# Performance work log

Hardware: AMD Instinct MI355X
Metric: run time of the kernel (lower is better)

Reference implementation:

```python
import jax, jax.numpy as jnp
import numpy as np

VOCAB, EMB, HID, OUT = 32000, 512, 1024, 2
B, T = 64, 512


def setup_inputs() -> dict:
    key = jax.random.key(0)
    ks = jax.random.split(key, 12)
    def xavier(k, shape):
        fan_in, fan_out = shape
        lim = np.sqrt(6.0 / (fan_in + fan_out)).astype(np.float32)
        return jax.random.uniform(k, shape, jnp.float32, -lim, lim)
    x = jax.random.randint(ks[0], (B, T), 0, VOCAB, dtype=jnp.int32)
    emb = jax.random.uniform(ks[1], (VOCAB, EMB), jnp.float32, -0.1, 0.1)
    inp = {
        "x": x,
        "emb": emb,
        "Wxi": xavier(ks[2], (EMB, HID)), "Whi": xavier(ks[3], (HID, HID)), "bi": jnp.zeros((HID,), jnp.float32),
        "Wxf": xavier(ks[4], (EMB, HID)), "Whf": xavier(ks[5], (HID, HID)), "bf": jnp.zeros((HID,), jnp.float32),
        "Wxc": xavier(ks[6], (EMB, HID)), "Whc": xavier(ks[7], (HID, HID)), "bc": jnp.zeros((HID,), jnp.float32),
        "Wxo": xavier(ks[8], (EMB, HID)), "Who": xavier(ks[9], (HID, HID)), "bo": jnp.zeros((HID,), jnp.float32),
        "Why": xavier(ks[10], (HID, OUT)), "by": jnp.zeros((OUT,), jnp.float32),
    }
    return inp


def reference(x, emb, Wxi, Whi, bi, Wxf, Whf, bf, Wxc, Whc, bc, Wxo, Who, bo, Why, by):
    # Embedding lookup: [B, T, E]
    xe = emb[x]
    # Precompute input projections for all 4 gates in one batched contraction each.
    # Stack Wx matrices -> [E, 4H]; gates_x: [T, B, 4H] (time-major for scan)
    Wx = jnp.concatenate([Wxi, Wxf, Wxc, Wxo], axis=1)          # [E, 4H]
    Wh = jnp.concatenate([Whi, Whf, Whc, Who], axis=1)          # [H, 4H]
    b = jnp.concatenate([bi, bf, bc, bo], axis=0)               # [4H]
    gates_x = jnp.einsum('bte,eg->tbg', xe, Wx)                  # [T, B, 4H]
    H = Whi.shape[0]

    def step(carry, gx):
        h, c = carry
        g = gx + h @ Wh + b                                      # [B, 4H]
        i = jax.nn.sigmoid(g[:, 0 * H:1 * H])
        f = jax.nn.sigmoid(g[:, 1 * H:2 * H])
        gg = jnp.tanh(g[:, 2 * H:3 * H])
        o = jax.nn.sigmoid(g[:, 3 * H:4 * H])
        c = f * c + i * gg
        h = o * jnp.tanh(c)
        return (h, c), None

    h0 = jnp.zeros((x.shape[0], H), xe.dtype)
    c0 = jnp.zeros((x.shape[0], H), xe.dtype)
    (h, c), _ = jax.lax.scan(step, (h0, c0), gates_x)
    # dropout is identity in eval mode
    return h @ Why + by
```

## Files before the change

### kernel.cpp

```cpp
#include <hip/hip_runtime.h>

#define TT 512
#define BB 64
#define EMB 512
#define HID 1024
#define K4 1536
#define NBLK 256
#define THREADS 256

typedef __bf16 bf16x8 __attribute__((ext_vector_type(8)));
typedef float f32x4 __attribute__((ext_vector_type(4)));

__device__ __forceinline__ unsigned short f2bf(float f) {
    union { float f; unsigned u; } v; v.f = f;
    unsigned u = v.u;
    unsigned r = u + 0x7FFFu + ((u >> 16) & 1u);
    return (unsigned short)(r >> 16);
}

__global__ void zero_kernel(unsigned* p, int n) {
    int i = blockIdx.x * 256 + threadIdx.x;
    if (i < n) p[i] = 0u;
}

__global__ void xe_kernel(const int* __restrict__ x, const float* __restrict__ emb,
                          unsigned short* __restrict__ xe_all) {
    int rowid = blockIdx.x;
    int t = rowid >> 6, b = rowid & 63;
    int idx = x[b * TT + t];
    float4 v = ((const float4*)(emb + (long)idx * EMB))[threadIdx.x];
    ushort4 o;
    o.x = f2bf(v.x); o.y = f2bf(v.y); o.z = f2bf(v.z); o.w = f2bf(v.w);
    ((ushort4*)(xe_all + (long)rowid * EMB))[threadIdx.x] = o;
}

__global__ void wpack_kernel(const float* __restrict__ Wxi, const float* __restrict__ Whi,
                             const float* __restrict__ Wxf, const float* __restrict__ Whf,
                             const float* __restrict__ Wxc, const float* __restrict__ Whc,
                             const float* __restrict__ Wxo, const float* __restrict__ Who,
                             unsigned short* __restrict__ Wpack) {
    const float* Wx[4] = {Wxi, Wxf, Wxc, Wxo};
    const float* Wh[4] = {Whi, Whf, Whc, Who};
    int n0 = (blockIdx.x & 15) << 8;
    int k0 = (blockIdx.x >> 4) << 3;
    int g = n0 >> 10, col0 = n0 & 1023;
    const float* base = (k0 < 512) ? (Wx[g] + (long)k0 * HID + col0)
                                   : (Wh[g] + (long)(k0 - 512) * HID + col0);
    int tid = threadIdx.x;
    union { unsigned short s[8]; uint4 v; } out;
#pragma unroll
    for (int i = 0; i < 8; ++i) out.s[i] = f2bf(base[(long)i * HID + tid]);
    *(uint4*)(Wpack + (long)(n0 + tid) * K4 + k0) = out.v;
}

#define MFMA(a, b, c) __builtin_amdgcn_mfma_f32_16x16x32_bf16((a), (b), (c), 0, 0, 0)

__launch_bounds__(THREADS, 1)
__global__ void lstm_kernel(const unsigned short* __restrict__ xe_all,
                            const unsigned short* __restrict__ Wpack,
                            unsigned short* __restrict__ hbuf,
                            float* __restrict__ hfinal,
                            unsigned* __restrict__ arrive,
                            const float* __restrict__ bi_p, const float* __restrict__ bf_p,
                            const float* __restrict__ bc_p, const float* __restrict__ bo_p) {
    __shared__ unsigned short Wlds[32 * 1536];
    __shared__ float partials[4][32][34];

    const int tid = threadIdx.x;
    const int wave = tid >> 6, lane = tid & 63;
    const int quad = lane >> 4, r16 = lane & 15;
    const int ks4 = wave;
    const int bid = blockIdx.x;
    const int half = bid & 1;
    const int j0 = (bid >> 1) * 8;

#pragma unroll
    for (int i = 0; i < 24; ++i) {
        int gidx = tid + i * THREADS;
        int c = gidx / 192, q = gidx % 192;
        int n = ((c >> 3) << 10) + j0 + (c & 7);
        *(uint4*)(&Wlds[(c * 192 + (q ^ (c & 7))) * 8]) =
            *(const uint4*)(Wpack + (long)n * K4 + q * 8);
    }
    const int b_loc = tid >> 3, jj = tid & 7;
    const int b_ = half * 32 + b_loc;
    float rb0 = bi_p[j0 + jj], rb1 = bf_p[j0 + jj], rb2 = bc_p[j0 + jj], rb3 = bo_p[j0 + jj];
    float c_state = 0.f;
    __syncthreads();

    const f32x4 zf = {0.f, 0.f, 0.f, 0.f};
    const int row0 = half * 32 + r16;
    const int s0 = r16 & 7;

    for (int t = 0; t < TT; ++t) {
        const unsigned short* xe_t = xe_all + (long)t * (BB * EMB);
        const unsigned short* hb = hbuf + (t & 1) * (BB * HID);

        f32x4 acc00 = zf, acc01 = zf, acc10 = zf, acc11 = zf;

        {
            uint4 xa[4][2];
#pragma unroll
            for (int i = 0; i < 4; ++i) {
                int k = ks4 * 128 + i * 32 + quad * 8;
                xa[i][0] = *(const uint4*)(xe_t + (long)row0 * EMB + k);
                xa[i][1] = *(const uint4*)(xe_t + (long)(row0 + 16) * EMB + k);
            }
#pragma unroll
            for (int i = 0; i < 4; ++i) {
                int bk = (ks4 * 128 + i * 32 + quad * 8) >> 3;
                bf16x8 b0 = *(const bf16x8*)(&Wlds[(r16 * 192 + (bk ^ s0)) * 8]);
                bf16x8 b1 = *(const bf16x8*)(&Wlds[((16 + r16) * 192 + (bk ^ s0)) * 8]);
                bf16x8 a0 = __builtin_bit_cast(bf16x8, xa[i][0]);
                bf16x8 a1 = __builtin_bit_cast(bf16x8, xa[i][1]);
                acc00 = MFMA(a0, b0, acc00); acc01 = MFMA(a0, b1, acc01);
                acc10 = MFMA(a1, b0, acc10); acc11 = MFMA(a1, b1, acc11);
            }
        }

        if (t > 0 && wave == 0) {
            const unsigned* fp = &arrive[((t - 1) * 16 + half * 8 + (lane & 7)) * 16];
            while (!__all(__hip_atomic_load(fp, __ATOMIC_RELAXED,
                                            __HIP_MEMORY_SCOPE_AGENT) >= 16u))
                __builtin_amdgcn_s_sleep(2);
        }
        __syncthreads();

        {
            uint4 ha[8][2];
#pragma unroll
            for (int i = 0; i < 8; ++i) {
                const unsigned short* p0 = hb + (long)row0 * HID + ks4 * 256 + i * 32 + quad * 8;
                const unsigned short* p1 = p0 + 16 * HID;
                asm volatile("global_load_dwordx4 %0, %1, off sc1" : "=v"(ha[i][0]) : "v"(p0));
                asm volatile("global_load_dwordx4 %0, %1, off sc1" : "=v"(ha[i][1]) : "v"(p1));
            }
            asm volatile("s_waitcnt vmcnt(0)" ::: "memory");
#pragma unroll
            for (int i = 0; i < 8; ++i) {
                int bk = (512 + ks4 * 256 + i * 32 + quad * 8) >> 3;
                bf16x8 b0 = *(const bf16x8*)(&Wlds[(r16 * 192 + (bk ^ s0)) * 8]);
                bf16x8 b1 = *(const bf16x8*)(&Wlds[((16 + r16) * 192 + (bk ^ s0)) * 8]);
                bf16x8 a0 = __builtin_bit_cast(bf16x8, ha[i][0]);
                bf16x8 a1 = __builtin_bit_cast(bf16x8, ha[i][1]);
                acc00 = MFMA(a0, b0, acc00); acc01 = MFMA(a0, b1, acc01);
                acc10 = MFMA(a1, b0, acc10); acc11 = MFMA(a1, b1, acc11);
            }
        }

        {
            int pr0 = quad * 4;
#pragma unroll
            for (int rr = 0; rr < 4; ++rr) {
                partials[ks4][pr0 + rr][r16]           = acc00[rr];
                partials[ks4][pr0 + rr][16 + r16]      = acc01[rr];
                partials[ks4][pr0 + 16 + rr][r16]      = acc10[rr];
                partials[ks4][pr0 + 16 + rr][16 + r16] = acc11[rr];
            }
        }
        __syncthreads();

        float gi = 0.f, gf = 0.f, gc = 0.f, go = 0.f;
#pragma unroll
        for (int w = 0; w < 4; ++w) {
            gi += partials[w][b_loc][jj];
            gf += partials[w][b_loc][8 + jj];
            gc += partials[w][b_loc][16 + jj];
            go += partials[w][b_loc][24 + jj];
        }
        gi += rb0; gf += rb1; gc += rb2; go += rb3;
        float si = 1.f / (1.f + __expf(-gi));
        float sf = 1.f / (1.f + __expf(-gf));
        float so = 1.f / (1.f + __expf(-go));
        float e2 = __expf(2.f * gc); float tc = (e2 - 1.f) / (e2 + 1.f);
        float c = sf * c_state + si * tc;
        c_state = c;
        float e2c = __expf(2.f * c); float th = (e2c - 1.f) / (e2c + 1.f);
        float h = so * th;

        unsigned short hv = f2bf(h);
        const unsigned short* hop = hbuf + ((t + 1) & 1) * (BB * HID) + b_ * HID + j0 + jj;
        asm volatile("global_store_short %0, %1, off sc1" :: "v"(hop), "v"(hv) : "memory");
        if (t == TT - 1) hfinal[b_ * HID + j0 + jj] = h;
        asm volatile("s_waitcnt vmcnt(0)" ::: "memory");
        __syncthreads();
        if (tid == 0)
            __hip_atomic_fetch_add(&arrive[(t * 16 + half * 8 + ((bid >> 1) & 7)) * 16], 1u,
                                   __ATOMIC_RELAXED, __HIP_MEMORY_SCOPE_AGENT);
    }
}

__global__ void out_kernel(const float* __restrict__ hfinal, const float* __restrict__ Why,
                           const float* __restrict__ by, float* __restrict__ y) {
    int gw = blockIdx.x * 4 + (threadIdx.x >> 6);
    int lane = threadIdx.x & 63;
    int b = gw >> 1, o = gw & 1;
    float s = 0.f;
    for (int k = lane; k < HID; k += 64) s += hfinal[b * HID + k] * Why[k * 2 + o];
#pragma unroll
    for (int off = 32; off; off >>= 1) s += __shfl_down(s, off);
    if (lane == 0) y[b * 2 + o] = s + by[o];
}

extern "C" void kernel_launch(void* const* d_in, const int* in_sizes, int n_in,
                              void* d_out, int out_size, void* d_ws, size_t ws_size,
                              hipStream_t stream) {
    const int*   x   = (const int*)d_in[0];
    const float* emb = (const float*)d_in[1];
    const float* Wxi = (const float*)d_in[2];
    const float* Whi = (const float*)d_in[3];
    const float* bi  = (const float*)d_in[4];
    const float* Wxf = (const float*)d_in[5];
    const float* Whf = (const float*)d_in[6];
    const float* bfp = (const float*)d_in[7];
    const float* Wxc = (const float*)d_in[8];
    const float* Whc = (const float*)d_in[9];
    const float* bc  = (const float*)d_in[10];
    const float* Wxo = (const float*)d_in[11];
    const float* Who = (const float*)d_in[12];
    const float* bo  = (const float*)d_in[13];
    const float* Why = (const float*)d_in[14];
    const float* by  = (const float*)d_in[15];
    float* y = (float*)d_out;

    char* ws = (char*)d_ws;
    unsigned short* Wpack  = (unsigned short*)ws;
    unsigned short* xe_all = (unsigned short*)(ws + 12582912);
    unsigned short* hbuf   = (unsigned short*)(ws + 12582912 + 33554432);
    unsigned*       arrive = (unsigned*)(ws + 12582912 + 33554432 + 262144);
    float*          hfinal = (float*)(ws + 12582912 + 33554432 + 262144 + 524288);

    zero_kernel<<<768, 256, 0, stream>>>((unsigned*)hbuf, 196608);
    wpack_kernel<<<3072, 256, 0, stream>>>(Wxi, Whi, Wxf, Whf, Wxc, Whc, Wxo, Who, Wpack);
    xe_kernel<<<32768, 128, 0, stream>>>(x, emb, xe_all);

    const unsigned short* xe_p = xe_all;
    const unsigned short* Wp_p = Wpack;
    unsigned short* hb_p = hbuf;
    float* hf_p = hfinal;
    unsigned* ar_p = arrive;
    void* args[] = {&xe_p, &Wp_p, &hb_p, &hf_p, &ar_p,
                    (void*)&bi, (void*)&bfp, (void*)&bc, (void*)&bo};
    hipLaunchCooperativeKernel((void*)lstm_kernel, dim3(NBLK), dim3(THREADS), args, 0, stream);

    out_kernel<<<32, 256, 0, stream>>>(hfinal, Why, by, y);
}
```

Measured before the change: 2.733 ms.

## Replace per-step atomic arrival counters with replicated monotonic flag tags

Swaps the per-timestep atomic-add arrival counters for per-block monotonic step tags, written as plain stores. Each producer block replicates its tag into 16 sets so that waiters spread their polling across different cache lines. Each waiting lane polls two producer tags with sc1 loads and a shorter sleep. This removes atomic contention and the per-timestep counter memory, shrinking the zeroed region. The cost is more polling loads per wait and extra stores per block per step, plus reliance on store ordering for the h visibility.

```diff
diff --git a/kernel.cpp b/kernel.cpp
--- a/kernel.cpp
+++ b/kernel.cpp
@@ -60,7 +60,7 @@
                             const unsigned short* __restrict__ Wpack,
                             unsigned short* __restrict__ hbuf,
                             float* __restrict__ hfinal,
-                            unsigned* __restrict__ arrive,
+                            unsigned* __restrict__ tags,
                             const float* __restrict__ bi_p, const float* __restrict__ bf_p,
                             const float* __restrict__ bc_p, const float* __restrict__ bo_p) {
     __shared__ unsigned short Wlds[32 * 1536];
@@ -72,7 +72,9 @@
     const int ks4 = wave;
     const int bid = blockIdx.x;
     const int half = bid & 1;
-    const int j0 = (bid >> 1) * 8;
+    const int pidx = bid >> 1;
+    const int j0 = pidx * 8;
+    const int set = pidx & 15;
 
 #pragma unroll
     for (int i = 0; i < 24; ++i) {
@@ -92,6 +94,9 @@
     const int row0 = half * 32 + r16;
     const int s0 = r16 & 7;
 
+    const unsigned* tpl0 = tags + (((long)half * 16 + set) * 128 + lane) * 16;
+    const unsigned* tpl1 = tpl0 + 64 * 16;
+
     for (int t = 0; t < TT; ++t) {
         const unsigned short* xe_t = xe_all + (long)t * (BB * EMB);
         const unsigned short* hb = hbuf + (t & 1) * (BB * HID);
@@ -119,10 +124,16 @@
         }
 
         if (t > 0 && wave == 0) {
-            const unsigned* fp = &arrive[((t - 1) * 16 + half * 8 + (lane & 7)) * 16];
-            while (!__all(__hip_atomic_load(fp, __ATOMIC_RELAXED,
-                                            __HIP_MEMORY_SCOPE_AGENT) >= 16u))
-                __builtin_amdgcn_s_sleep(2);
+            const unsigned tgt = (unsigned)t;
+            for (;;) {
+                unsigned a, b;
+                asm volatile("global_load_dword %0, %2, off sc1\n\t"
+                             "global_load_dword %1, %3, off sc1\n\t"
+                             "s_waitcnt vmcnt(0)"
+                             : "=v"(a), "=v"(b) : "v"(tpl0), "v"(tpl1));
+                if (__all(a >= tgt && b >= tgt)) break;
+                __builtin_amdgcn_s_sleep(1);
+            }
         }
         __syncthreads();
 
@@ -184,9 +195,11 @@
         if (t == TT - 1) hfinal[b_ * HID + j0 + jj] = h;
         asm volatile("s_waitcnt vmcnt(0)" ::: "memory");
         __syncthreads();
-        if (tid == 0)
-            __hip_atomic_fetch_add(&arrive[(t * 16 + half * 8 + ((bid >> 1) & 7)) * 16], 1u,
-                                   __ATOMIC_RELAXED, __HIP_MEMORY_SCOPE_AGENT);
+        if (tid < 16) {
+            unsigned* tp = (unsigned*)tags + (((long)half * 16 + tid) * 128 + pidx) * 16;
+            unsigned val = (unsigned)(t + 1);
+            asm volatile("global_store_dword %0, %1, off sc1" :: "v"(tp), "v"(val) : "memory");
+        }
     }
 }
 
@@ -227,10 +240,10 @@
     unsigned short* Wpack  = (unsigned short*)ws;
     unsigned short* xe_all = (unsigned short*)(ws + 12582912);
     unsigned short* hbuf   = (unsigned short*)(ws + 12582912 + 33554432);
-    unsigned*       arrive = (unsigned*)(ws + 12582912 + 33554432 + 262144);
-    float*          hfinal = (float*)(ws + 12582912 + 33554432 + 262144 + 524288);
-
-    zero_kernel<<<768, 256, 0, stream>>>((unsigned*)hbuf, 196608);
+    unsigned*       tags   = (unsigned*)(ws + 12582912 + 33554432 + 262144);
+    float*          hfinal = (float*)(ws + 12582912 + 33554432 + 262144 + 262144);
+
+    zero_kernel<<<512, 256, 0, stream>>>((unsigned*)hbuf, 131072);
     wpack_kernel<<<3072, 256, 0, stream>>>(Wxi, Whi, Wxf, Whf, Wxc, Whc, Wxo, Who, Wpack);
     xe_kernel<<<32768, 128, 0, stream>>>(x, emb, xe_all);
 
@@ -238,8 +251,8 @@
     const unsigned short* Wp_p = Wpack;
     unsigned short* hb_p = hbuf;
     float* hf_p = hfinal;
-    unsigned* ar_p = arrive;
-    void* args[] = {&xe_p, &Wp_p, &hb_p, &hf_p, &ar_p,
+    unsigned* tg_p = tags;
+    void* args[] = {&xe_p, &Wp_p, &hb_p, &hf_p, &tg_p,
                     (void*)&bi, (void*)&bfp, (void*)&bc, (void*)&bo};
     hipLaunchCooperativeKernel((void*)lstm_kernel, dim3(NBLK), dim3(THREADS), args, 0, stream);
 
```

Result: slower. 2.790 ms (+2.1%).
